# Optimization experiments

Measured on AMD Instinct MI355X. Metric: run time of the kernel, lower is better.

The kernel has to match this reference:

```python
import jax, jax.numpy as jnp
from jax import lax
import numpy as np

B, T, D, H, N_MID = 1024, 256, 64, 128, 1000000

def setup_inputs() -> dict:
    key = jax.random.key(0)
    ks = jax.random.split(key, 7)
    item_his = jax.random.randint(ks[0], (B, T), 0, N_MID)
    seq_lens = jax.random.randint(ks[1], (B,), 0, T)
    embedding = jax.random.normal(ks[2], (N_MID, D), dtype=jnp.float32) * 0.05
    gate_kernel = jax.random.normal(ks[3], (D + H, 2 * H), dtype=jnp.float32) * 0.05
    gate_bias = jax.random.normal(ks[4], (2 * H,), dtype=jnp.float32) * 0.05
    cand_kernel = jax.random.normal(ks[5], (D + H, H), dtype=jnp.float32) * 0.05
    cand_bias = jax.random.normal(ks[6], (H,), dtype=jnp.float32) * 0.05
    return {"item_his": item_his, "seq_lens": seq_lens, "embedding": embedding,
            "gate_kernel": gate_kernel, "gate_bias": gate_bias,
            "cand_kernel": cand_kernel, "cand_bias": cand_bias}

def _gru_final_state(x, seq_lens, gate_kernel, gate_bias, cand_kernel, cand_bias):
    # x: [B, T, D]; TF GRUCell math with dynamic_rnn sequence_length masking.
    b, t, d = x.shape
    h_dim = cand_bias.shape[0]
    mask = jnp.arange(t)[None, :] < seq_lens[:, None]  # [B, T]

    def step(h, inp):
        xt, m = inp  # xt: [B, D], m: [B]
        xh = jnp.concatenate([xt, h], axis=-1)              # [B, D+H]
        g = jax.nn.sigmoid(xh @ gate_kernel + gate_bias)    # [B, 2H]
        r, u = jnp.split(g, 2, axis=-1)
        xrh = jnp.concatenate([xt, r * h], axis=-1)
        c = jnp.tanh(xrh @ cand_kernel + cand_bias)
        h_new = u * h + (1.0 - u) * c
        h = jnp.where(m[:, None], h_new, h)  # copy-through past seq end
        return h, None

    h0 = jnp.zeros((b, h_dim), dtype=x.dtype)
    xs = (jnp.swapaxes(x, 0, 1), jnp.swapaxes(mask, 0, 1))
    hT, _ = lax.scan(step, h0, xs)
    return hT

def reference(item_his, seq_lens, embedding, gate_kernel, gate_bias, cand_kernel, cand_bias):
    x = embedding[item_his]  # [B, T, D]
    user_eb = _gru_final_state(x, seq_lens, gate_kernel, gate_bias, cand_kernel, cand_bias)
    return user_eb
```

## Files before the change

### kernel.cpp

```cpp
#include <hip/hip_runtime.h>


#define T_   256
#define D_   64
#define H_   128
#define SROW 208

typedef _Float16 half8_t  __attribute__((ext_vector_type(8)));
typedef _Float16 half4_t  __attribute__((ext_vector_type(4)));
typedef float    floatx4  __attribute__((ext_vector_type(4)));

__device__ __forceinline__ float fast_sigmoid(float x) {
    return __builtin_amdgcn_rcpf(1.f + __expf(-x));
}
__device__ __forceinline__ float fast_tanh(float s) {
    s = fminf(fmaxf(s, -15.f), 15.f);
    return 1.f - 2.f * __builtin_amdgcn_rcpf(1.f + __expf(2.f * s));
}

__global__ __launch_bounds__(256, 1) void gru_mfma(
    const int* __restrict__ item_his,
    const int* __restrict__ seq_lens,
    const float* __restrict__ emb,
    const float* __restrict__ Wg,
    const float* __restrict__ bg,
    const float* __restrict__ Wc,
    const float* __restrict__ bc,
    float* __restrict__ out)
{
    __shared__ __align__(16) _Float16 XT[T_][4][D_];
    __shared__ __align__(16) _Float16 XA[16][SROW];
    __shared__ __align__(16) _Float16 XC[16][SROW];

    const int tid  = threadIdx.x;
    const int w    = tid >> 6;
    const int lane = tid & 63;
    const int row0 = blockIdx.x * 4;

    const int bq = lane >> 4;
    const int bn = lane & 15;

    half8_t BG0[2][6], BG1[2][6], BC6[2][6];
    #pragma unroll
    for (int j = 0; j < 2; ++j) {
        const int col = (2 * w + j) * 16 + bn;
        #pragma unroll
        for (int kt = 0; kt < 6; ++kt) {
            half8_t f0, f1, fc;
            #pragma unroll
            for (int i = 0; i < 8; ++i) {
                const int k = kt * 32 + bq * 8 + i;
                f0[i] = (_Float16)Wg[k * 256 + col];
                f1[i] = (_Float16)Wg[k * 256 + 128 + col];
                fc[i] = (_Float16)Wc[k * 128 + col];
            }
            BG0[j][kt] = f0; BG1[j][kt] = f1; BC6[j][kt] = fc;
        }
    }

    float bgR[2], bgU[2], bcC[2];
    #pragma unroll
    for (int j = 0; j < 2; ++j) {
        const int col = (2 * w + j) * 16 + bn;
        bgR[j] = bg[col];
        bgU[j] = bg[128 + col];
        bcC[j] = bc[col];
    }

    int len[4];
    #pragma unroll
    for (int r = 0; r < 4; ++r) len[r] = seq_lens[row0 + r];
    const int maxlen = max(max(len[0], len[1]), max(len[2], len[3]));

    {
        unsigned* pa = (unsigned*)&XA[0][0];
        unsigned* pc = (unsigned*)&XC[0][0];
        for (int i = tid; i < 16 * SROW / 2; i += 256) { pa[i] = 0u; pc[i] = 0u; }
    }

    {
        const int nq = maxlen << 6;
        for (int i0 = tid; i0 < nq; i0 += 2048) {
            int id[8];
            #pragma unroll
            for (int b = 0; b < 8; ++b) {
                const int i = i0 + (b << 8);
                if (i < nq) id[b] = item_his[(row0 + ((i >> 4) & 3)) * T_ + (i >> 6)];
            }
            float4 v[8];
            #pragma unroll
            for (int b = 0; b < 8; ++b) {
                const int i = i0 + (b << 8);
                if (i < nq)
                    v[b] = *(const float4*)&emb[(size_t)id[b] * D_ + ((i & 15) << 2)];
            }
            #pragma unroll
            for (int b = 0; b < 8; ++b) {
                const int i = i0 + (b << 8);
                if (i < nq) {
                    half4_t hv;
                    hv[0] = (_Float16)v[b].x; hv[1] = (_Float16)v[b].y;
                    hv[2] = (_Float16)v[b].z; hv[3] = (_Float16)v[b].w;
                    *(half4_t*)&XT[i >> 6][(i >> 4) & 3][(i & 15) << 2] = hv;
                }
            }
        }
    }
    __syncthreads();

    if (tid < 64) {
        const half4_t v = *(const half4_t*)&XT[0][tid >> 4][(tid & 15) * 4];
        *(half4_t*)&XA[tid >> 4][(tid & 15) * 4] = v;
    }
    float h[2][4] = {{0.f,0.f,0.f,0.f},{0.f,0.f,0.f,0.f}};
    __syncthreads();

    for (int t = 0; t < maxlen; ++t) {
        half8_t af[6];
        #pragma unroll
        for (int kt = 0; kt < 6; ++kt)
            af[kt] = *(const half8_t*)&XA[bn][kt * 32 + bq * 8];

        floatx4 aR[2], aU[2], aCx[2];
        #pragma unroll
        for (int j = 0; j < 2; ++j) {
            aR[j]  = (floatx4){bgR[j], bgR[j], bgR[j], bgR[j]};
            aU[j]  = (floatx4){bgU[j], bgU[j], bgU[j], bgU[j]};
            aCx[j] = (floatx4){bcC[j], bcC[j], bcC[j], bcC[j]};
        }
        #pragma unroll
        for (int kt = 0; kt < 6; ++kt) {
            #pragma unroll
            for (int j = 0; j < 2; ++j) {
                aR[j] = __builtin_amdgcn_mfma_f32_16x16x32_f16(af[kt], BG0[j][kt], aR[j], 0, 0, 0);
                aU[j] = __builtin_amdgcn_mfma_f32_16x16x32_f16(af[kt], BG1[j][kt], aU[j], 0, 0, 0);
                if (kt < 2)
                    aCx[j] = __builtin_amdgcn_mfma_f32_16x16x32_f16(af[kt], BC6[j][kt], aCx[j], 0, 0, 0);
            }
        }
        if (lane < 16) {
            #pragma unroll
            for (int j = 0; j < 2; ++j)
                #pragma unroll
                for (int r = 0; r < 4; ++r) {
                    const float rg = fast_sigmoid(aR[j][r]);
                    XC[r][(2 * w + j) * 16 + lane] = (_Float16)(rg * h[j][r]);
                }
        }
        __syncthreads();

        if (tid < 64) {
            const half4_t v = *(const half4_t*)&XT[t + 1][tid >> 4][(tid & 15) * 4];
            *(half4_t*)&XA[tid >> 4][(tid & 15) * 4] = v;
        }
        half8_t cf[4];
        #pragma unroll
        for (int kk = 0; kk < 4; ++kk)
            cf[kk] = *(const half8_t*)&XC[bn][kk * 32 + bq * 8];
        floatx4 aC[2] = {aCx[0], aCx[1]};
        #pragma unroll
        for (int kk = 0; kk < 4; ++kk)
            #pragma unroll
            for (int j = 0; j < 2; ++j)
                aC[j] = __builtin_amdgcn_mfma_f32_16x16x32_f16(cf[kk], BC6[j][kk + 2], aC[j], 0, 0, 0);

        if (lane < 16) {
            #pragma unroll
            for (int j = 0; j < 2; ++j)
                #pragma unroll
                for (int r = 0; r < 4; ++r) {
                    const float ug = fast_sigmoid(aU[j][r]);
                    const float c  = fast_tanh(aC[j][r]);
                    const float hn = c + ug * (h[j][r] - c);
                    if (t < len[r]) h[j][r] = hn;
                    XA[r][64 + (2 * w + j) * 16 + lane] = (_Float16)h[j][r];
                }
        }
        __syncthreads();
    }

    if (lane < 16) {
        #pragma unroll
        for (int j = 0; j < 2; ++j)
            #pragma unroll
            for (int r = 0; r < 4; ++r)
                out[(row0 + r) * H_ + (2 * w + j) * 16 + lane] = h[j][r];
    }
}

extern "C" void kernel_launch(void* const* d_in, const int* in_sizes, int n_in,
                              void* d_out, int out_size, void* d_ws, size_t ws_size,
                              hipStream_t stream) {
    const int*   item_his = (const int*)d_in[0];
    const int*   seq_lens = (const int*)d_in[1];
    const float* emb      = (const float*)d_in[2];
    const float* Wg       = (const float*)d_in[3];
    const float* bg       = (const float*)d_in[4];
    const float* Wc       = (const float*)d_in[5];
    const float* bc       = (const float*)d_in[6];
    float*       out      = (float*)d_out;

    gru_mfma<<<256, 256, 0, stream>>>(item_his, seq_lens, emb, Wg, bg, Wc, bc, out);
}
```

Baseline: 595.2 us.

## Split MFMA accumulator chains and read x directly from embedding tile

The x-part A-fragments are now loaded straight from the staged XT tile, with a zero row for the padding rows, so the per-step copy of x into XA is dropped. The recurrent MFMA chains are split into two independent accumulators each to shorten the dependency latency. The update-gate MFMAs are moved after the reset-gate epilogue so they can overlap with it. This adds extra accumulator registers and some float additions per step.

After: 605.5 us. Within noise of the previous version (+1.7%).

```diff
diff --git a/kernel.cpp b/kernel.cpp
--- a/kernel.cpp
+++ b/kernel.cpp
@@ -31,6 +31,7 @@
     __shared__ __align__(16) _Float16 XT[T_][4][D_];
     __shared__ __align__(16) _Float16 XA[16][SROW];
     __shared__ __align__(16) _Float16 XC[16][SROW];
+    __shared__ __align__(16) _Float16 ZROW[64];
 
     const int tid  = threadIdx.x;
     const int w    = tid >> 6;
@@ -76,6 +77,7 @@
         unsigned* pa = (unsigned*)&XA[0][0];
         unsigned* pc = (unsigned*)&XC[0][0];
         for (int i = tid; i < 16 * SROW / 2; i += 256) { pa[i] = 0u; pc[i] = 0u; }
+        if (tid < 32) ((unsigned*)ZROW)[tid] = 0u;
     }
 
     {
@@ -106,20 +108,21 @@
             }
         }
     }
-    __syncthreads();
-
-    if (tid < 64) {
-        const half4_t v = *(const half4_t*)&XT[0][tid >> 4][(tid & 15) * 4];
-        *(half4_t*)&XA[tid >> 4][(tid & 15) * 4] = v;
-    }
     float h[2][4] = {{0.f,0.f,0.f,0.f},{0.f,0.f,0.f,0.f}};
     __syncthreads();
 
     for (int t = 0; t < maxlen; ++t) {
-        half8_t af[6];
-        #pragma unroll
-        for (int kt = 0; kt < 6; ++kt)
-            af[kt] = *(const half8_t*)&XA[bn][kt * 32 + bq * 8];
+        half8_t ax[2];
+        {
+            const _Float16* p0 = (bn < 4) ? &XT[t][bn][bq * 8]      : &ZROW[bq * 8];
+            const _Float16* p1 = (bn < 4) ? &XT[t][bn][32 + bq * 8] : &ZROW[bq * 8];
+            ax[0] = *(const half8_t*)p0;
+            ax[1] = *(const half8_t*)p1;
+        }
+        half8_t ah[4];
+        #pragma unroll
+        for (int kk = 0; kk < 4; ++kk)
+            ah[kk] = *(const half8_t*)&XA[bn][64 + kk * 32 + bq * 8];
 
         floatx4 aR[2], aU[2], aCx[2];
         #pragma unroll
@@ -127,50 +130,62 @@
             aR[j]  = (floatx4){bgR[j], bgR[j], bgR[j], bgR[j]};
             aU[j]  = (floatx4){bgU[j], bgU[j], bgU[j], bgU[j]};
             aCx[j] = (floatx4){bcC[j], bcC[j], bcC[j], bcC[j]};
-        }
-        #pragma unroll
-        for (int kt = 0; kt < 6; ++kt) {
-            #pragma unroll
-            for (int j = 0; j < 2; ++j) {
-                aR[j] = __builtin_amdgcn_mfma_f32_16x16x32_f16(af[kt], BG0[j][kt], aR[j], 0, 0, 0);
-                aU[j] = __builtin_amdgcn_mfma_f32_16x16x32_f16(af[kt], BG1[j][kt], aU[j], 0, 0, 0);
-                if (kt < 2)
-                    aCx[j] = __builtin_amdgcn_mfma_f32_16x16x32_f16(af[kt], BC6[j][kt], aCx[j], 0, 0, 0);
-            }
+            #pragma unroll
+            for (int kt = 0; kt < 2; ++kt) {
+                aR[j]  = __builtin_amdgcn_mfma_f32_16x16x32_f16(ax[kt], BG0[j][kt], aR[j],  0, 0, 0);
+                aU[j]  = __builtin_amdgcn_mfma_f32_16x16x32_f16(ax[kt], BG1[j][kt], aU[j],  0, 0, 0);
+                aCx[j] = __builtin_amdgcn_mfma_f32_16x16x32_f16(ax[kt], BC6[j][kt], aCx[j], 0, 0, 0);
+            }
+        }
+        floatx4 aRb[2], aUb[2];
+        #pragma unroll
+        for (int j = 0; j < 2; ++j) {
+            aR[j]  = __builtin_amdgcn_mfma_f32_16x16x32_f16(ah[0], BG0[j][2], aR[j], 0, 0, 0);
+            aRb[j] = __builtin_amdgcn_mfma_f32_16x16x32_f16(ah[1], BG0[j][3],
+                         (floatx4){0.f,0.f,0.f,0.f}, 0, 0, 0);
+            aR[j]  = __builtin_amdgcn_mfma_f32_16x16x32_f16(ah[2], BG0[j][4], aR[j],  0, 0, 0);
+            aRb[j] = __builtin_amdgcn_mfma_f32_16x16x32_f16(ah[3], BG0[j][5], aRb[j], 0, 0, 0);
         }
         if (lane < 16) {
             #pragma unroll
             for (int j = 0; j < 2; ++j)
                 #pragma unroll
                 for (int r = 0; r < 4; ++r) {
-                    const float rg = fast_sigmoid(aR[j][r]);
+                    const float rg = fast_sigmoid(aR[j][r] + aRb[j][r]);
                     XC[r][(2 * w + j) * 16 + lane] = (_Float16)(rg * h[j][r]);
                 }
         }
+        #pragma unroll
+        for (int j = 0; j < 2; ++j) {
+            aU[j]  = __builtin_amdgcn_mfma_f32_16x16x32_f16(ah[0], BG1[j][2], aU[j], 0, 0, 0);
+            aUb[j] = __builtin_amdgcn_mfma_f32_16x16x32_f16(ah[1], BG1[j][3],
+                         (floatx4){0.f,0.f,0.f,0.f}, 0, 0, 0);
+            aU[j]  = __builtin_amdgcn_mfma_f32_16x16x32_f16(ah[2], BG1[j][4], aU[j],  0, 0, 0);
+            aUb[j] = __builtin_amdgcn_mfma_f32_16x16x32_f16(ah[3], BG1[j][5], aUb[j], 0, 0, 0);
+        }
         __syncthreads();
 
-        if (tid < 64) {
-            const half4_t v = *(const half4_t*)&XT[t + 1][tid >> 4][(tid & 15) * 4];
-            *(half4_t*)&XA[tid >> 4][(tid & 15) * 4] = v;
-        }
         half8_t cf[4];
         #pragma unroll
         for (int kk = 0; kk < 4; ++kk)
             cf[kk] = *(const half8_t*)&XC[bn][kk * 32 + bq * 8];
-        floatx4 aC[2] = {aCx[0], aCx[1]};
-        #pragma unroll
-        for (int kk = 0; kk < 4; ++kk)
-            #pragma unroll
-            for (int j = 0; j < 2; ++j)
-                aC[j] = __builtin_amdgcn_mfma_f32_16x16x32_f16(cf[kk], BC6[j][kk + 2], aC[j], 0, 0, 0);
-
+
+        floatx4 aC[2] = {aCx[0], aCx[1]}, aCb[2];
+        #pragma unroll
+        for (int j = 0; j < 2; ++j) {
+            aC[j]  = __builtin_amdgcn_mfma_f32_16x16x32_f16(cf[0], BC6[j][2], aC[j], 0, 0, 0);
+            aCb[j] = __builtin_amdgcn_mfma_f32_16x16x32_f16(cf[1], BC6[j][3],
+                         (floatx4){0.f,0.f,0.f,0.f}, 0, 0, 0);
+            aC[j]  = __builtin_amdgcn_mfma_f32_16x16x32_f16(cf[2], BC6[j][4], aC[j],  0, 0, 0);
+            aCb[j] = __builtin_amdgcn_mfma_f32_16x16x32_f16(cf[3], BC6[j][5], aCb[j], 0, 0, 0);
+        }
         if (lane < 16) {
             #pragma unroll
             for (int j = 0; j < 2; ++j)
                 #pragma unroll
                 for (int r = 0; r < 4; ++r) {
-                    const float ug = fast_sigmoid(aU[j][r]);
-                    const float c  = fast_tanh(aC[j][r]);
+                    const float ug = fast_sigmoid(aU[j][r] + aUb[j][r]);
+                    const float c  = fast_tanh(aC[j][r] + aCb[j][r]);
                     const float hn = c + ug * (h[j][r] - c);
                     if (t < len[r]) h[j][r] = hn;
                     XA[r][64 + (2 * w + j) * 16 + lane] = (_Float16)h[j][r];
```

## Process two row groups per block and prefetch embeddings inside the recurrence

Applied to the files above, without the earlier changes.

Each block now handles eight sequences as two independent groups of four, interleaving their MFMA chains to hide the per-step latency. The up-front embedding gather into shared memory is replaced by per-step register prefetching two steps ahead, overlapping gather latency with compute. Half as many blocks are launched, so fewer CUs are used. The loop length now follows the maximum of eight sequence lengths.

New measurement: 773.6 us. 30.0% more time.

```diff
diff --git a/kernel.cpp b/kernel.cpp
--- a/kernel.cpp
+++ b/kernel.cpp
@@ -7,7 +7,6 @@
 #define SROW 208
 
 typedef _Float16 half8_t  __attribute__((ext_vector_type(8)));
-typedef _Float16 half4_t  __attribute__((ext_vector_type(4)));
 typedef float    floatx4  __attribute__((ext_vector_type(4)));
 
 __device__ __forceinline__ float fast_sigmoid(float x) {
@@ -28,14 +27,13 @@
     const float* __restrict__ bc,
     float* __restrict__ out)
 {
-    __shared__ __align__(16) _Float16 XT[T_][4][D_];
-    __shared__ __align__(16) _Float16 XA[16][SROW];
-    __shared__ __align__(16) _Float16 XC[16][SROW];
+    __shared__ __align__(16) _Float16 XA[2][16][SROW];
+    __shared__ __align__(16) _Float16 XC[2][16][SROW];
 
     const int tid  = threadIdx.x;
     const int w    = tid >> 6;
     const int lane = tid & 63;
-    const int row0 = blockIdx.x * 4;
+    const int row0 = blockIdx.x * 8;
 
     const int bq = lane >> 4;
     const int bn = lane & 15;
@@ -58,133 +56,159 @@
         }
     }
 
-    float bgR[2], bgU[2], bcC[2];
+    floatx4 cbR[2], cbU[2], cbC[2];
     #pragma unroll
     for (int j = 0; j < 2; ++j) {
         const int col = (2 * w + j) * 16 + bn;
-        bgR[j] = bg[col];
-        bgU[j] = bg[128 + col];
-        bcC[j] = bc[col];
-    }
-
-    int len[4];
-    #pragma unroll
-    for (int r = 0; r < 4; ++r) len[r] = seq_lens[row0 + r];
-    const int maxlen = max(max(len[0], len[1]), max(len[2], len[3]));
+        const float r_ = bg[col], u_ = bg[128 + col], c_ = bc[col];
+        cbR[j] = (floatx4){r_, r_, r_, r_};
+        cbU[j] = (floatx4){u_, u_, u_, u_};
+        cbC[j] = (floatx4){c_, c_, c_, c_};
+    }
+
+    int len[2][4];
+    int maxlen = 0;
+    #pragma unroll
+    for (int g = 0; g < 2; ++g)
+        #pragma unroll
+        for (int r = 0; r < 4; ++r) {
+            len[g][r] = seq_lens[row0 + 4 * g + r];
+            maxlen = max(maxlen, len[g][r]);
+        }
 
     {
-        unsigned* pa = (unsigned*)&XA[0][0];
-        unsigned* pc = (unsigned*)&XC[0][0];
-        for (int i = tid; i < 16 * SROW / 2; i += 256) { pa[i] = 0u; pc[i] = 0u; }
-    }
-
-    {
-        const int nq = maxlen << 6;
-        for (int i0 = tid; i0 < nq; i0 += 2048) {
-            int id[8];
-            #pragma unroll
-            for (int b = 0; b < 8; ++b) {
-                const int i = i0 + (b << 8);
-                if (i < nq) id[b] = item_his[(row0 + ((i >> 4) & 3)) * T_ + (i >> 6)];
+        unsigned* pa = (unsigned*)&XA[0][0][0];
+        unsigned* pc = (unsigned*)&XC[0][0][0];
+        for (int i = tid; i < 2 * 16 * SROW / 2; i += 256) { pa[i] = 0u; pc[i] = 0u; }
+    }
+    __syncthreads();
+
+    int   ib[2];
+    float xA[2] = {0.f, 0.f}, xB[2] = {0.f, 0.f};
+    int   iN[2] = {0, 0},     iM[2] = {0, 0};
+    #pragma unroll
+    for (int g = 0; g < 2; ++g) ib[g] = (row0 + 4 * g + w) * T_;
+
+    if (maxlen > 0) {
+        #pragma unroll
+        for (int g = 0; g < 2; ++g) {
+            const int i0 = item_his[ib[g] + 0];
+            const int i1 = item_his[ib[g] + 1];
+            iN[g] = item_his[ib[g] + 2];
+            const float x0 = emb[(size_t)i0 * D_ + lane];
+            xA[g] = emb[(size_t)i1 * D_ + lane];
+            XA[g][w][lane] = (_Float16)x0;
+        }
+    }
+    float h[2][2][4];
+    float u[2][2][4];
+    #pragma unroll
+    for (int g = 0; g < 2; ++g)
+        #pragma unroll
+        for (int j = 0; j < 2; ++j)
+            #pragma unroll
+            for (int r = 0; r < 4; ++r) { h[g][j][r] = 0.f; u[g][j][r] = 0.f; }
+    floatx4 pAC[2][2];
+    __syncthreads();
+
+    auto step = [&](int t, float (&xNow)[2], float (&xNew)[2],
+                    int (&jNow)[2], int (&jNew)[2]) {
+        #pragma unroll
+        for (int g = 0; g < 2; ++g) {
+            xNew[g] = emb[(size_t)jNow[g] * D_ + lane];
+            const int t3 = (t + 3 < T_) ? (t + 3) : (T_ - 1);
+            jNew[g] = item_his[ib[g] + t3];
+        }
+        half8_t af[2][6];
+        #pragma unroll
+        for (int g = 0; g < 2; ++g)
+            #pragma unroll
+            for (int kt = 0; kt < 6; ++kt)
+                af[g][kt] = *(const half8_t*)&XA[g][bn][kt * 32 + bq * 8];
+
+        floatx4 aR[2][2], aU[2][2];
+        #pragma unroll
+        for (int g = 0; g < 2; ++g)
+            #pragma unroll
+            for (int j = 0; j < 2; ++j) {
+                floatx4 r_ = cbR[j], u_ = cbU[j], cx = cbC[j];
+                #pragma unroll
+                for (int kt = 0; kt < 6; ++kt) {
+                    r_ = __builtin_amdgcn_mfma_f32_16x16x32_f16(af[g][kt], BG0[j][kt], r_, 0, 0, 0);
+                    u_ = __builtin_amdgcn_mfma_f32_16x16x32_f16(af[g][kt], BG1[j][kt], u_, 0, 0, 0);
+                    if (kt < 2)
+                        cx = __builtin_amdgcn_mfma_f32_16x16x32_f16(af[g][kt], BC6[j][kt], cx, 0, 0, 0);
+                }
+                aR[g][j] = r_; aU[g][j] = u_; pAC[g][j] = cx;
             }
-            float4 v[8];
-            #pragma unroll
-            for (int b = 0; b < 8; ++b) {
-                const int i = i0 + (b << 8);
-                if (i < nq)
-                    v[b] = *(const float4*)&emb[(size_t)id[b] * D_ + ((i & 15) << 2)];
+        if (lane < 16) {
+            #pragma unroll
+            for (int g = 0; g < 2; ++g)
+                #pragma unroll
+                for (int j = 0; j < 2; ++j)
+                    #pragma unroll
+                    for (int r = 0; r < 4; ++r) {
+                        const float rg = fast_sigmoid(aR[g][j][r]);
+                        u[g][j][r]     = fast_sigmoid(aU[g][j][r]);
+                        XC[g][r][(2 * w + j) * 16 + lane] = (_Float16)(rg * h[g][j][r]);
+                    }
+        }
+        __syncthreads();
+
+        half8_t cf[2][4];
+        #pragma unroll
+        for (int g = 0; g < 2; ++g)
+            #pragma unroll
+            for (int kk = 0; kk < 4; ++kk)
+                cf[g][kk] = *(const half8_t*)&XC[g][bn][kk * 32 + bq * 8];
+
+        floatx4 aC[2][2];
+        #pragma unroll
+        for (int g = 0; g < 2; ++g)
+            #pragma unroll
+            for (int j = 0; j < 2; ++j) {
+                floatx4 c_ = pAC[g][j];
+                #pragma unroll
+                for (int kk = 0; kk < 4; ++kk)
+                    c_ = __builtin_amdgcn_mfma_f32_16x16x32_f16(cf[g][kk], BC6[j][kk + 2], c_, 0, 0, 0);
+                aC[g][j] = c_;
             }
-            #pragma unroll
-            for (int b = 0; b < 8; ++b) {
-                const int i = i0 + (b << 8);
-                if (i < nq) {
-                    half4_t hv;
-                    hv[0] = (_Float16)v[b].x; hv[1] = (_Float16)v[b].y;
-                    hv[2] = (_Float16)v[b].z; hv[3] = (_Float16)v[b].w;
-                    *(half4_t*)&XT[i >> 6][(i >> 4) & 3][(i & 15) << 2] = hv;
-                }
-            }
-        }
-    }
-    __syncthreads();
-
-    if (tid < 64) {
-        const half4_t v = *(const half4_t*)&XT[0][tid >> 4][(tid & 15) * 4];
-        *(half4_t*)&XA[tid >> 4][(tid & 15) * 4] = v;
-    }
-    float h[2][4] = {{0.f,0.f,0.f,0.f},{0.f,0.f,0.f,0.f}};
-    __syncthreads();
-
-    for (int t = 0; t < maxlen; ++t) {
-        half8_t af[6];
-        #pragma unroll
-        for (int kt = 0; kt < 6; ++kt)
-            af[kt] = *(const half8_t*)&XA[bn][kt * 32 + bq * 8];
-
-        floatx4 aR[2], aU[2], aCx[2];
-        #pragma unroll
-        for (int j = 0; j < 2; ++j) {
-            aR[j]  = (floatx4){bgR[j], bgR[j], bgR[j], bgR[j]};
-            aU[j]  = (floatx4){bgU[j], bgU[j], bgU[j], bgU[j]};
-            aCx[j] = (floatx4){bcC[j], bcC[j], bcC[j], bcC[j]};
-        }
-        #pragma unroll
-        for (int kt = 0; kt < 6; ++kt) {
-            #pragma unroll
-            for (int j = 0; j < 2; ++j) {
-                aR[j] = __builtin_amdgcn_mfma_f32_16x16x32_f16(af[kt], BG0[j][kt], aR[j], 0, 0, 0);
-                aU[j] = __builtin_amdgcn_mfma_f32_16x16x32_f16(af[kt], BG1[j][kt], aU[j], 0, 0, 0);
-                if (kt < 2)
-                    aCx[j] = __builtin_amdgcn_mfma_f32_16x16x32_f16(af[kt], BC6[j][kt], aCx[j], 0, 0, 0);
-            }
-        }
+        XA[0][w][lane] = (_Float16)xNow[0];
+        XA[1][w][lane] = (_Float16)xNow[1];
+
         if (lane < 16) {
             #pragma unroll
+            for (int g = 0; g < 2; ++g)
+                #pragma unroll
+                for (int j = 0; j < 2; ++j)
+                    #pragma unroll
+                    for (int r = 0; r < 4; ++r) {
+                        const float c  = fast_tanh(aC[g][j][r]);
+                        const float hn = c + u[g][j][r] * (h[g][j][r] - c);
+                        if (t < len[g][r]) h[g][j][r] = hn;
+                        XA[g][r][64 + (2 * w + j) * 16 + lane] = (_Float16)h[g][j][r];
+                    }
+        }
+        __syncthreads();
+    };
+
+    int t = 0;
+    while (t < maxlen) {
+        step(t, xA, xB, iN, iM);
+        ++t;
+        if (t >= maxlen) break;
+        step(t, xB, xA, iM, iN);
+        ++t;
+    }
+
+    if (lane < 16) {
+        #pragma unroll
+        for (int g = 0; g < 2; ++g)
+            #pragma unroll
             for (int j = 0; j < 2; ++j)
                 #pragma unroll
-                for (int r = 0; r < 4; ++r) {
-                    const float rg = fast_sigmoid(aR[j][r]);
-                    XC[r][(2 * w + j) * 16 + lane] = (_Float16)(rg * h[j][r]);
-                }
-        }
-        __syncthreads();
-
-        if (tid < 64) {
-            const half4_t v = *(const half4_t*)&XT[t + 1][tid >> 4][(tid & 15) * 4];
-            *(half4_t*)&XA[tid >> 4][(tid & 15) * 4] = v;
-        }
-        half8_t cf[4];
-        #pragma unroll
-        for (int kk = 0; kk < 4; ++kk)
-            cf[kk] = *(const half8_t*)&XC[bn][kk * 32 + bq * 8];
-        floatx4 aC[2] = {aCx[0], aCx[1]};
-        #pragma unroll
-        for (int kk = 0; kk < 4; ++kk)
-            #pragma unroll
-            for (int j = 0; j < 2; ++j)
-                aC[j] = __builtin_amdgcn_mfma_f32_16x16x32_f16(cf[kk], BC6[j][kk + 2], aC[j], 0, 0, 0);
-
-        if (lane < 16) {
-            #pragma unroll
-            for (int j = 0; j < 2; ++j)
-                #pragma unroll
-                for (int r = 0; r < 4; ++r) {
-                    const float ug = fast_sigmoid(aU[j][r]);
-                    const float c  = fast_tanh(aC[j][r]);
-                    const float hn = c + ug * (h[j][r] - c);
-                    if (t < len[r]) h[j][r] = hn;
-                    XA[r][64 + (2 * w + j) * 16 + lane] = (_Float16)h[j][r];
-                }
-        }
-        __syncthreads();
-    }
-
-    if (lane < 16) {
-        #pragma unroll
-        for (int j = 0; j < 2; ++j)
-            #pragma unroll
-            for (int r = 0; r < 4; ++r)
-                out[(row0 + r) * H_ + (2 * w + j) * 16 + lane] = h[j][r];
+                for (int r = 0; r < 4; ++r)
+                    out[(row0 + 4 * g + r) * H_ + (2 * w + j) * 16 + lane] = h[g][j][r];
     }
 }
 
@@ -200,5 +224,5 @@
     const float* bc       = (const float*)d_in[6];
     float*       out      = (float*)d_out;
 
-    gru_mfma<<<256, 256, 0, stream>>>(item_his, seq_lens, emb, Wg, bg, Wc, bc, out);
-}
+    gru_mfma<<<128, 256, 0, stream>>>(item_his, seq_lens, emb, Wg, bg, Wc, bc, out);
+}
```
